# Optimization experiments

Hardware: AMD Instinct MI355X
Metric: run time of the kernel (lower is better)

The kernel has to match this reference:

```python
import jax, jax.numpy as jnp
import numpy as np

EPS = 1e-8

def _cos_loss(a, b):
    # faithful to torch cos_loss: norm = sqrt(sum(x*x)), x / (norm + 1e-8)
    a_norm = jnp.sqrt(jnp.sum(a * a, axis=1, keepdims=True))
    b_norm = jnp.sqrt(jnp.sum(b * b, axis=1, keepdims=True))
    a_n = a / (a_norm + EPS)
    b_n = b / (b_norm + EPS)
    cossim = jnp.sum(a_n * b_n, axis=1)
    return jnp.mean(1.0 - cossim)

def setup_inputs() -> dict:
    key = jax.random.key(0)
    k1, k2, k3 = jax.random.split(key, 3)
    shape = (1, 768, 64, 64)  # [n, c_cat(block2 VGG16 feats), h, w]
    a = jax.random.normal(k1, shape, dtype=jnp.float32)
    b = jax.random.normal(k2, shape, dtype=jnp.float32)
    d = jax.random.normal(k3, shape, dtype=jnp.float32)
    return {"a": a, "b": b, "d": d}

def reference(a, b, d):
    n, c, h, w = a.shape
    hw = h * w
    a_flat = a.reshape(n, c, hw)   # [n, c, hw]
    b_flat = b.reshape(n, c, hw)   # [n, c, h2w2]
    d_flat = d.reshape(n, c, hw)
    # normalize exactly as argmin_cos_distance: sqrt(sum + 1e-8) then /(norm + 1e-8)
    b_norm = jnp.sqrt(jnp.sum(b_flat * b_flat, axis=1, keepdims=True) + EPS)
    b_n = b_flat / (b_norm + EPS)
    a_norm = jnp.sqrt(jnp.sum(a_flat * a_flat, axis=1, keepdims=True) + EPS)
    a_n = a_flat / (a_norm + EPS)
    # cosine distance matrix [n, hw, h2w2]
    d_mat = 1.0 - jnp.einsum('ncp,ncq->npq', a_n, b_n)
    z_best = jnp.argmin(d_mat, axis=2)  # [n, hw]
    # gather matched style features from d
    idx = jnp.broadcast_to(z_best[:, None, :], (n, c, hw))
    target_feats = jnp.take_along_axis(d_flat, idx, axis=2)  # [n, c, hw]
    # NNFM loss between rendered feats and matched style feats (score is detached)
    loss = _cos_loss(a_flat, target_feats)
    z_new = target_feats.reshape(n, c, h, w)
    return (loss, z_new, z_best)
```

## Files before the change

### kernel.cpp

```cpp
#include <hip/hip_runtime.h>
#include <math.h>

#define EPS  1e-8f
#define C    768
#define HW   4096
#define NKB  24
#define NNB  12
#define NBN  32
#define TAU  0.016f
#define NCH_NEW 12
#define NCH_OLD 48

typedef float  floatx4 __attribute__((ext_vector_type(4)));
typedef short  shortx8 __attribute__((ext_vector_type(8)));
typedef unsigned short ushort_t;
typedef unsigned int   uint_t;
typedef __attribute__((address_space(1))) uint_t as1_uint;
typedef __attribute__((address_space(3))) uint_t as3_uint;

__device__ __forceinline__ ushort_t f2bf(float v) {
    uint_t u = __float_as_uint(v);
    uint_t r = (u + 0x7FFFu + ((u >> 16) & 1u)) >> 16;
    return (ushort_t)r;
}
__device__ __forceinline__ void async_cp16(const ushort_t* g, ushort_t* l) {
    __builtin_amdgcn_global_load_lds((const as1_uint*)g, (as3_uint*)l, 16, 0, 0);
}

__global__ __launch_bounds__(256) void prep_kernel(
    const float* __restrict__ a, const float* __restrict__ b,
    const float* __restrict__ d,
    ushort_t* __restrict__ Ah, ushort_t* __restrict__ Bh,
    float* __restrict__ dT, float* __restrict__ bT,
    float* __restrict__ nbp2, float* __restrict__ out)
{
    __shared__ float tile[64][65];
    const int t = threadIdx.x;
    const int p0 = blockIdx.x * 64;
    const int c0 = blockIdx.y * 64;
    const int x = t & 63, y4 = t >> 6;
    const int pl = t >> 2, g = t & 3;
    const int pg = p0 + pl;
    const int sw = (pg >> 1) & 3;

    if (blockIdx.x == 0 && blockIdx.y == 0 && t == 0) out[0] = 0.f;

#pragma unroll
    for (int i = 0; i < 16; ++i) {
        int c = y4 * 16 + i;
        tile[c][x] = d[(size_t)(c0 + c) * HW + p0 + x];
    }
    __syncthreads();
#pragma unroll
    for (int i = 0; i < 16; ++i) {
        int p = y4 * 16 + i;
        dT[(size_t)(p0 + p) * C + c0 + x] = tile[x][p];
    }
    __syncthreads();

#pragma unroll
    for (int i = 0; i < 16; ++i) {
        int c = y4 * 16 + i;
        tile[c][x] = b[(size_t)(c0 + c) * HW + p0 + x];
    }
    __syncthreads();
#pragma unroll
    for (int i = 0; i < 16; ++i) {
        int p = y4 * 16 + i;
        bT[(size_t)(p0 + p) * C + c0 + x] = tile[x][p];
    }
#pragma unroll
    for (int h = 0; h < 2; ++h) {
        const int kb = (c0 >> 5) + h;
        uint_t w[4];
#pragma unroll
        for (int u = 0; u < 4; ++u) {
            ushort_t lo = f2bf(tile[h * 32 + g * 8 + 2 * u][pl]);
            ushort_t hi = f2bf(tile[h * 32 + g * 8 + 2 * u + 1][pl]);
            w[u] = (uint_t)lo | ((uint_t)hi << 16);
        }
        uint4* oh = (uint4*)(Bh + ((size_t)kb * HW + pg) * 32);
        oh[g ^ sw] = make_uint4(w[0], w[1], w[2], w[3]);
    }
    if (t < 64) {
        float s = 0.f;
#pragma unroll
        for (int c = 0; c < 64; ++c) { float v = tile[c][t]; s += v * v; }
        nbp2[blockIdx.y * HW + p0 + t] = s;
    }
    __syncthreads();

#pragma unroll
    for (int i = 0; i < 16; ++i) {
        int c = y4 * 16 + i;
        tile[c][x] = a[(size_t)(c0 + c) * HW + p0 + x];
    }
    __syncthreads();
#pragma unroll
    for (int h = 0; h < 2; ++h) {
        const int kb = (c0 >> 5) + h;
        uint_t w[4];
#pragma unroll
        for (int u = 0; u < 4; ++u) {
            ushort_t lo = f2bf(tile[h * 32 + g * 8 + 2 * u][pl]);
            ushort_t hi = f2bf(tile[h * 32 + g * 8 + 2 * u + 1][pl]);
            w[u] = (uint_t)lo | ((uint_t)hi << 16);
        }
        uint4* oh = (uint4*)(Ah + ((size_t)kb * HW + pg) * 32);
        oh[g ^ sw] = make_uint4(w[0], w[1], w[2], w[3]);
    }
}

__global__ __launch_bounds__(256, 4) void gemm_mfma_kernel(
    const ushort_t* __restrict__ Ah, const ushort_t* __restrict__ Bh,
    const float* __restrict__ nbp2,
    float* __restrict__ pv1, int* __restrict__ pi1,
    float* __restrict__ pv2, int* __restrict__ pi2)
{
    __shared__ __align__(16) char smem[33280];
    ushort_t* sA0 = (ushort_t*)smem;
    ushort_t* sB0 = (ushort_t*)(smem + 8192);
    ushort_t* sA1 = (ushort_t*)(smem + 16384);
    ushort_t* sB1 = (ushort_t*)(smem + 24576);
    float*    nb_s = (float*)(smem + 32768);

    const int tid  = threadIdx.x;
    const int lane = tid & 63;
    const int wave = tid >> 6;
    const int wm = wave >> 1, wn = wave & 1;
    const int bm = blockIdx.x, bn = blockIdx.y;
    const int l15 = lane & 15, l4 = lane >> 4;
    const int swz = (l15 >> 1) & 3;

    floatx4 acc[4][4];
#pragma unroll
    for (int i = 0; i < 4; ++i)
#pragma unroll
        for (int j = 0; j < 4; ++j) acc[i][j] = (floatx4){0.f, 0.f, 0.f, 0.f};

    auto stage = [&](int kb, ushort_t* dA, ushort_t* dB) {
        const size_t aoff = (size_t)(kb * HW + bm * 128) * 32 + tid * 8;
        const size_t boff = (size_t)(kb * HW + bn * 128) * 32 + tid * 8;
        async_cp16(Ah + aoff,        dA + tid * 8);
        async_cp16(Ah + aoff + 2048, dA + tid * 8 + 2048);
        async_cp16(Bh + boff,        dB + tid * 8);
        async_cp16(Bh + boff + 2048, dB + tid * 8 + 2048);
    };
    auto compute = [&](const ushort_t* pA, const ushort_t* pB) {
        shortx8 af[4], bf_[4];
#pragma unroll
        for (int i = 0; i < 4; ++i)
            af[i] = *(const shortx8*)&pA[((wm * 4 + i) * 16 + l15) * 32 + ((l4 ^ swz) * 8)];
#pragma unroll
        for (int j = 0; j < 4; ++j)
            bf_[j] = *(const shortx8*)&pB[((wn * 4 + j) * 16 + l15) * 32 + ((l4 ^ swz) * 8)];
#pragma unroll
        for (int i = 0; i < 4; ++i)
#pragma unroll
            for (int j = 0; j < 4; ++j)
                acc[i][j] = __builtin_amdgcn_mfma_f32_16x16x32_bf16(af[i], bf_[j], acc[i][j], 0, 0, 0);
    };

    stage(0, sA0, sB0);
    if (tid < 128) {
        float s = 0.f;
        int q = bn * 128 + tid;
#pragma unroll
        for (int ch = 0; ch < NNB; ++ch) s += nbp2[ch * HW + q];
        nb_s[tid] = 1.0f / (sqrtf(s + EPS) + EPS);
    }
    __syncthreads();

    for (int kb = 0; kb < NKB; kb += 2) {
        stage(kb + 1, sA1, sB1);
        compute(sA0, sB0);
        __syncthreads();
        if (kb + 2 < NKB) stage(kb + 2, sA0, sB0);
        compute(sA1, sB1);
        __syncthreads();
    }

    float rnb[4];
#pragma unroll
    for (int j = 0; j < 4; ++j)
        rnb[j] = nb_s[wn * 64 + j * 16 + l15];

    float* lv1 = (float*)smem;
    int*   li1 = (int*)(smem + 1024);
    float* lv2 = (float*)(smem + 2048);
    int*   li2 = (int*)(smem + 3072);

#pragma unroll
    for (int i = 0; i < 4; ++i) {
#pragma unroll
        for (int r = 0; r < 4; ++r) {
            float v1 = -INFINITY, v2 = -INFINITY; int i1 = 0, i2 = 0;
#pragma unroll
            for (int j = 0; j < 4; ++j) {
                float sv = acc[i][j][r] * rnb[j];
                int q = bn * 128 + wn * 64 + j * 16 + l15;
                if (sv > v1) { v2 = v1; i2 = i1; v1 = sv; i1 = q; }
                else if (sv > v2) { v2 = sv; i2 = q; }
            }
#pragma unroll
            for (int m = 1; m < 16; m <<= 1) {
                float ov1 = __shfl_xor(v1, m, 64);
                int   oi1 = __shfl_xor(i1, m, 64);
                float ov2 = __shfl_xor(v2, m, 64);
                int   oi2 = __shfl_xor(i2, m, 64);
                if (ov1 > v1 || (ov1 == v1 && oi1 < i1)) {
                    if (v1 > ov2 || (v1 == ov2 && i1 < oi2)) { v2 = v1; i2 = i1; }
                    else { v2 = ov2; i2 = oi2; }
                    v1 = ov1; i1 = oi1;
                } else if (ov1 > v2 || (ov1 == v2 && oi1 < i2)) {
                    v2 = ov1; i2 = oi1;
                }
            }
            if (l15 == 0) {
                int pl = wm * 64 + i * 16 + l4 * 4 + r;
                lv1[pl * 2 + wn] = v1; li1[pl * 2 + wn] = i1;
                lv2[pl * 2 + wn] = v2; li2[pl * 2 + wn] = i2;
            }
        }
    }
    __syncthreads();
    if (tid < 128) {
        float v1 = lv1[tid * 2],     v2 = lv2[tid * 2];
        int   i1 = li1[tid * 2],     i2 = li2[tid * 2];
        float w1 = lv1[tid * 2 + 1], w2 = lv2[tid * 2 + 1];
        int   j1 = li1[tid * 2 + 1], j2 = li2[tid * 2 + 1];
        if (w1 > v1 || (w1 == v1 && j1 < i1)) {
            if (v1 > w2 || (v1 == w2 && i1 < j2)) { v2 = v1; i2 = i1; }
            else { v2 = w2; i2 = j2; }
            v1 = w1; i1 = j1;
        } else if (w1 > v2 || (w1 == v2 && j1 < i2)) {
            v2 = w1; i2 = j1;
        }
        int p = bm * 128 + tid;
        pv1[p * NBN + bn] = v1; pi1[p * NBN + bn] = i1;
        pv2[p * NBN + bn] = v2; pi2[p * NBN + bn] = i2;
    }
}

__global__ __launch_bounds__(256) void reduce_recheck_kernel(
    const float* __restrict__ a, const float* __restrict__ b,
    const float* __restrict__ bT, int bt_ok,
    const float* __restrict__ pv1, const int* __restrict__ pi1,
    const float* __restrict__ pv2, const int* __restrict__ pi2,
    int* __restrict__ zb, float* __restrict__ out_zbest)
{
    const int wave = threadIdx.x >> 6, lane = threadIdx.x & 63;
    const int p = blockIdx.x * 4 + wave;
    const int tq = lane & 31;

    float v1, v2; int i1, cand;
    if (lane < 32) {
        v1 = pv1[p * NBN + tq]; i1 = pi1[p * NBN + tq]; v2 = pv2[p * NBN + tq];
        cand = i1;
    } else {
        v1 = -INFINITY; v2 = -INFINITY; i1 = 0x7fffffff;
        cand = pi2[p * NBN + tq];
    }
#pragma unroll
    for (int m = 1; m < 32; m <<= 1) {
        float ov1 = __shfl_xor(v1, m, 64);
        int   oi1 = __shfl_xor(i1, m, 64);
        float ov2 = __shfl_xor(v2, m, 64);
        if (ov1 > v1 || (ov1 == v1 && oi1 < i1)) {
            v2 = fmaxf(v1, ov2); v1 = ov1; i1 = oi1;
        } else {
            v2 = fmaxf(v2, ov1);
        }
    }
    v1 = __shfl(v1, 0, 64); v2 = __shfl(v2, 0, 64); i1 = __shfl(i1, 0, 64);

    if (v1 - v2 >= TAU) {
        if (lane == 0) { zb[p] = i1; out_zbest[p] = (float)i1; }
        return;
    }

    int q = cand;
    float dot = 0.f, b2 = 0.f;
    if (bt_ok) {
        const float* br = bT + (size_t)q * C;
        const float* ap = a + p;
#pragma unroll 4
        for (int c = 0; c < C; c += 4) {
            float4 bv = *(const float4*)(br + c);
            dot += ap[(size_t)c * HW] * bv.x + ap[(size_t)(c + 1) * HW] * bv.y
                 + ap[(size_t)(c + 2) * HW] * bv.z + ap[(size_t)(c + 3) * HW] * bv.w;
            b2  += bv.x * bv.x + bv.y * bv.y + bv.z * bv.z + bv.w * bv.w;
        }
    } else {
#pragma unroll 8
        for (int c = 0; c < C; ++c) {
            float av = a[c * HW + p];
            float bv = b[c * HW + q];
            dot += av * bv; b2 += bv * bv;
        }
    }
    float s = dot / (sqrtf(b2 + EPS) + EPS);
#pragma unroll
    for (int m = 1; m < 64; m <<= 1) {
        float os = __shfl_xor(s, m, 64);
        int   oq = __shfl_xor(q, m, 64);
        if (os > s || (os == s && oq < q)) { s = os; q = oq; }
    }
    if (lane == 0) { zb[p] = q; out_zbest[p] = (float)q; }
}

__global__ __launch_bounds__(256) void gather_loss_kernel(
    const float* __restrict__ a, const float* __restrict__ dT,
    const int* __restrict__ zb, float* __restrict__ out,
    float* __restrict__ pdot, float* __restrict__ pa2, float* __restrict__ pt2)
{
    __shared__ float tile[64][65];
    __shared__ int qs[64];
    const int t = threadIdx.x;
    const int p0 = blockIdx.x * 64;
    const int c0 = blockIdx.y * 64;
    if (t < 64) qs[t] = zb[p0 + t];
    __syncthreads();

    {
        const int pl = t >> 2, sub = t & 3;
        const float* src = dT + (size_t)qs[pl] * C + c0 + sub * 16;
        float4 v0 = *(const float4*)(src);
        float4 v1 = *(const float4*)(src + 4);
        float4 v2 = *(const float4*)(src + 8);
        float4 v3 = *(const float4*)(src + 12);
        float* dst = &tile[pl][sub * 16];
        dst[0] = v0.x; dst[1] = v0.y; dst[2]  = v0.z; dst[3]  = v0.w;
        dst[4] = v1.x; dst[5] = v1.y; dst[6]  = v1.z; dst[7]  = v1.w;
        dst[8] = v2.x; dst[9] = v2.y; dst[10] = v2.z; dst[11] = v2.w;
        dst[12] = v3.x; dst[13] = v3.y; dst[14] = v3.z; dst[15] = v3.w;
    }
    __syncthreads();

    const int p = t & 63, cg = t >> 6;
    float dot = 0.f, a2 = 0.f, t2 = 0.f;
#pragma unroll
    for (int i = 0; i < 16; ++i) {
        int cc = cg * 16 + i;
        float tv = tile[p][cc];
        float av = a[(size_t)(c0 + cc) * HW + p0 + p];
        out[1 + (size_t)(c0 + cc) * HW + p0 + p] = tv;
        dot += av * tv; a2 += av * av; t2 += tv * tv;
    }
    __shared__ float r1[256], r2[256], r3[256];
    r1[t] = dot; r2[t] = a2; r3[t] = t2;
    __syncthreads();
    if (t < 64) {
        dot = r1[t] + r1[t + 64] + r1[t + 128] + r1[t + 192];
        a2  = r2[t] + r2[t + 64] + r2[t + 128] + r2[t + 192];
        t2  = r3[t] + r3[t + 64] + r3[t + 128] + r3[t + 192];
        pdot[blockIdx.y * HW + p0 + t] = dot;
        pa2[blockIdx.y * HW + p0 + t]  = a2;
        pt2[blockIdx.y * HW + p0 + t]  = t2;
    }
}

__global__ __launch_bounds__(256) void loss_finalize_kernel(
    const float* __restrict__ pdot, const float* __restrict__ pa2,
    const float* __restrict__ pt2, float* __restrict__ out, int nch)
{
    int p = blockIdx.x * 256 + threadIdx.x;
    float dot = 0.f, a2 = 0.f, t2 = 0.f;
#pragma unroll 12
    for (int ch = 0; ch < nch; ++ch) {
        dot += pdot[ch * HW + p];
        a2  += pa2[ch * HW + p];
        t2  += pt2[ch * HW + p];
    }
    float cs = dot / ((sqrtf(a2) + EPS) * (sqrtf(t2) + EPS));
    float contrib = 1.f - cs;
    __shared__ float red[256];
    red[threadIdx.x] = contrib;
    __syncthreads();
    for (int s = 128; s > 0; s >>= 1) {
        if (threadIdx.x < s) red[threadIdx.x] += red[threadIdx.x + s];
        __syncthreads();
    }
    if (threadIdx.x == 0) atomicAdd(out, red[0] * (1.0f / HW));
}

__global__ __launch_bounds__(256) void bnorm_partial_fb_kernel(
    const float* __restrict__ b, float* __restrict__ nbp)
{
    int q = blockIdx.x * 256 + threadIdx.x;
    int c0 = blockIdx.y * 32;
    float s = 0.f;
#pragma unroll 8
    for (int c = c0; c < c0 + 32; ++c) { float v = b[c * HW + q]; s += v * v; }
    nbp[blockIdx.y * HW + q] = s;
}

__global__ __launch_bounds__(256) void bnorm_finalize_fb_kernel(
    const float* __restrict__ nbp, float* __restrict__ nb)
{
    int q = blockIdx.x * 256 + threadIdx.x;
    float s = 0.f;
#pragma unroll
    for (int ch = 0; ch < NKB; ++ch) s += nbp[ch * HW + q];
    nb[q] = sqrtf(s + EPS) + EPS;
}

__global__ __launch_bounds__(256) void gemm_argmax_fb_kernel(
    const float* __restrict__ A, const float* __restrict__ B,
    const float* __restrict__ nb,
    float* __restrict__ pval, int* __restrict__ pidx)
{
    __shared__ __align__(16) char smem[16384];
    float (*As)[128] = (float (*)[128])smem;
    float (*Bs)[128] = (float (*)[128])(smem + 4096);
    const int m0 = blockIdx.x * 128, q0 = blockIdx.y * 128;
    const int tid = threadIdx.x;
    const int tx = tid & 15, ty = tid >> 4;
    const int lr = tid >> 5, lc = (tid & 31) * 4;
    float acc[8][8] = {};
    for (int k0 = 0; k0 < C; k0 += 8) {
        *(float4*)&As[lr][lc] = *(const float4*)&A[(k0 + lr) * HW + m0 + lc];
        *(float4*)&Bs[lr][lc] = *(const float4*)&B[(k0 + lr) * HW + q0 + lc];
        __syncthreads();
#pragma unroll
        for (int kk = 0; kk < 8; ++kk) {
            float a8[8], b8[8];
            *(float4*)&a8[0] = *(float4*)&As[kk][ty * 8];
            *(float4*)&a8[4] = *(float4*)&As[kk][ty * 8 + 4];
            *(float4*)&b8[0] = *(float4*)&Bs[kk][tx * 8];
            *(float4*)&b8[4] = *(float4*)&Bs[kk][tx * 8 + 4];
#pragma unroll
            for (int i = 0; i < 8; ++i)
#pragma unroll
                for (int j = 0; j < 8; ++j) acc[i][j] += a8[i] * b8[j];
        }
        __syncthreads();
    }
    float nbv[8];
#pragma unroll
    for (int j = 0; j < 8; ++j) nbv[j] = nb[q0 + tx * 8 + j];
    float (*rv)[16] = (float (*)[16])smem;
    int   (*ri)[16] = (int   (*)[16])(smem + 8192);
#pragma unroll
    for (int i = 0; i < 8; ++i) {
        float bv = -INFINITY; int bi = 0;
#pragma unroll
        for (int j = 0; j < 8; ++j) {
            float s = acc[i][j] / nbv[j];
            int q = q0 + tx * 8 + j;
            if (s > bv) { bv = s; bi = q; }
        }
        rv[ty * 8 + i][tx] = bv;
        ri[ty * 8 + i][tx] = bi;
    }
    __syncthreads();
    if (tid < 128) {
        float bv = rv[tid][0]; int bi = ri[tid][0];
#pragma unroll
        for (int t = 1; t < 16; ++t) {
            float v = rv[tid][t]; int ii = ri[tid][t];
            if (v > bv || (v == bv && ii < bi)) { bv = v; bi = ii; }
        }
        pval[(m0 + tid) * NBN + blockIdx.y] = bv;
        pidx[(m0 + tid) * NBN + blockIdx.y] = bi;
    }
}

__global__ __launch_bounds__(256) void reduce_fb_kernel(
    const float* __restrict__ pval, const int* __restrict__ pidx,
    int* __restrict__ zb, float* __restrict__ out_zbest)
{
    int p = blockIdx.x * 256 + threadIdx.x;
    float bv = pval[p * NBN]; int bi = pidx[p * NBN];
#pragma unroll 8
    for (int t = 1; t < NBN; ++t) {
        float v = pval[p * NBN + t]; int ii = pidx[p * NBN + t];
        if (v > bv || (v == bv && ii < bi)) { bv = v; bi = ii; }
    }
    zb[p] = bi;
    out_zbest[p] = (float)bi;
}

__global__ __launch_bounds__(256) void gather_partial_kernel(
    const float* __restrict__ a, const float* __restrict__ d,
    const int* __restrict__ zb, float* __restrict__ out,
    float* __restrict__ pdot, float* __restrict__ pa2, float* __restrict__ pt2)
{
    int p = blockIdx.x * 256 + threadIdx.x;
    int ch = blockIdx.y;
    int c0 = ch * (C / NCH_OLD);
    int q = zb[p];
    float dot = 0.f, a2 = 0.f, t2 = 0.f;
#pragma unroll
    for (int c = c0; c < c0 + C / NCH_OLD; ++c) {
        float av = a[c * HW + p];
        float tv = d[c * HW + q];
        dot += av * tv; a2 += av * av; t2 += tv * tv;
        out[1 + c * HW + p] = tv;
    }
    pdot[ch * HW + p] = dot;
    pa2[ch * HW + p] = a2;
    pt2[ch * HW + p] = t2;
}

extern "C" void kernel_launch(void* const* d_in, const int* in_sizes, int n_in,
                              void* d_out, int out_size, void* d_ws, size_t ws_size,
                              hipStream_t stream) {
    const float* a = (const float*)d_in[0];
    const float* b = (const float*)d_in[1];
    const float* d = (const float*)d_in[2];
    float* out = (float*)d_out;
    float* out_zbest = out + 1 + (size_t)C * HW;

    char* ws = (char*)d_ws;
    size_t off = 0;
    auto alloc = [&](size_t bytes) { void* p = ws + off; off = (off + bytes + 255) & ~(size_t)255; return p; };

    const size_t PACK = (size_t)C * HW * 2;
    ushort_t* Ah = (ushort_t*)alloc(PACK);
    ushort_t* Bh = (ushort_t*)alloc(PACK);
    float* nbp = (float*)alloc((size_t)NKB * HW * 4);
    float* pv1 = (float*)alloc((size_t)HW * NBN * 4);
    int*   pi1 = (int*)alloc((size_t)HW * NBN * 4);
    float* pv2 = (float*)alloc((size_t)HW * NBN * 4);
    int*   pi2 = (int*)alloc((size_t)HW * NBN * 4);
    int*   zb  = (int*)alloc(HW * 4);
    float* pdot = (float*)alloc((size_t)NCH_NEW * HW * 4);
    float* pa2  = (float*)alloc((size_t)NCH_NEW * HW * 4);
    float* pt2  = (float*)alloc((size_t)NCH_NEW * HW * 4);
    float* dT  = (float*)alloc((size_t)C * HW * 4);
    float* bT  = (float*)alloc((size_t)C * HW * 4);
    bool fast = off <= ws_size;

    if (fast) {
        prep_kernel<<<dim3(HW / 64, C / 64), 256, 0, stream>>>(
            a, b, d, Ah, Bh, dT, bT, nbp, out);
        gemm_mfma_kernel<<<dim3(HW / 128, HW / 128), 256, 0, stream>>>(
            Ah, Bh, nbp, pv1, pi1, pv2, pi2);
        reduce_recheck_kernel<<<HW / 4, 256, 0, stream>>>(
            a, b, bT, 1, pv1, pi1, pv2, pi2, zb, out_zbest);
        gather_loss_kernel<<<dim3(HW / 64, NCH_NEW), 256, 0, stream>>>(
            a, dT, zb, out, pdot, pa2, pt2);
        loss_finalize_kernel<<<HW / 256, 256, 0, stream>>>(pdot, pa2, pt2, out, NCH_NEW);
    } else {
        off = 0;
        float* nb = (float*)alloc(HW * 4);
        nbp = (float*)alloc((size_t)NKB * HW * 4);
        pv1 = (float*)alloc((size_t)HW * NBN * 4);
        pi1 = (int*)alloc((size_t)HW * NBN * 4);
        zb  = (int*)alloc(HW * 4);
        float* pdot2 = (float*)alloc((size_t)NCH_OLD * HW * 4);
        float* pa22  = (float*)alloc((size_t)NCH_OLD * HW * 4);
        float* pt22  = (float*)alloc((size_t)NCH_OLD * HW * 4);
        hipMemsetAsync(d_out, 0, sizeof(float), stream);
        bnorm_partial_fb_kernel<<<dim3(HW / 256, NKB), 256, 0, stream>>>(b, nbp);
        bnorm_finalize_fb_kernel<<<HW / 256, 256, 0, stream>>>(nbp, nb);
        gemm_argmax_fb_kernel<<<dim3(HW / 128, HW / 128), 256, 0, stream>>>(a, b, nb, pv1, pi1);
        reduce_fb_kernel<<<HW / 256, 256, 0, stream>>>(pv1, pi1, zb, out_zbest);
        gather_partial_kernel<<<dim3(HW / 256, NCH_OLD), 256, 0, stream>>>(
            a, d, zb, out, pdot2, pa22, pt22);
        loss_finalize_kernel<<<HW / 256, 256, 0, stream>>>(pdot2, pa22, pt22, out, NCH_OLD);
    }
}
```

Baseline: 180.2 us.

## Vectorize prep transposes, swizzle GEMM block order, vectorize loss finalize

Result: no change. 180.0 us (-0.1%).

```diff
diff --git a/kernel.cpp b/kernel.cpp
--- a/kernel.cpp
+++ b/kernel.cpp
@@ -38,7 +38,8 @@
     const int t = threadIdx.x;
     const int p0 = blockIdx.x * 64;
     const int c0 = blockIdx.y * 64;
-    const int x = t & 63, y4 = t >> 6;
+    const int r16 = t >> 4;
+    const int q4  = (t & 15) * 4;
     const int pl = t >> 2, g = t & 3;
     const int pg = p0 + pl;
     const int sw = (pg >> 1) & 3;
@@ -46,28 +47,38 @@
     if (blockIdx.x == 0 && blockIdx.y == 0 && t == 0) out[0] = 0.f;
 
 #pragma unroll
-    for (int i = 0; i < 16; ++i) {
-        int c = y4 * 16 + i;
-        tile[c][x] = d[(size_t)(c0 + c) * HW + p0 + x];
-    }
-    __syncthreads();
-#pragma unroll
-    for (int i = 0; i < 16; ++i) {
-        int p = y4 * 16 + i;
-        dT[(size_t)(p0 + p) * C + c0 + x] = tile[x][p];
-    }
-    __syncthreads();
-
-#pragma unroll
-    for (int i = 0; i < 16; ++i) {
-        int c = y4 * 16 + i;
-        tile[c][x] = b[(size_t)(c0 + c) * HW + p0 + x];
-    }
-    __syncthreads();
-#pragma unroll
-    for (int i = 0; i < 16; ++i) {
-        int p = y4 * 16 + i;
-        bT[(size_t)(p0 + p) * C + c0 + x] = tile[x][p];
+    for (int pp = 0; pp < 4; ++pp) {
+        int c = pp * 16 + r16;
+        float4 v = *(const float4*)&d[(size_t)(c0 + c) * HW + p0 + q4];
+        tile[c][q4]     = v.x; tile[c][q4 + 1] = v.y;
+        tile[c][q4 + 2] = v.z; tile[c][q4 + 3] = v.w;
+    }
+    __syncthreads();
+#pragma unroll
+    for (int pp = 0; pp < 4; ++pp) {
+        int p = pp * 16 + r16;
+        float4 v;
+        v.x = tile[q4][p];     v.y = tile[q4 + 1][p];
+        v.z = tile[q4 + 2][p]; v.w = tile[q4 + 3][p];
+        *(float4*)&dT[(size_t)(p0 + p) * C + c0 + q4] = v;
+    }
+    __syncthreads();
+
+#pragma unroll
+    for (int pp = 0; pp < 4; ++pp) {
+        int c = pp * 16 + r16;
+        float4 v = *(const float4*)&b[(size_t)(c0 + c) * HW + p0 + q4];
+        tile[c][q4]     = v.x; tile[c][q4 + 1] = v.y;
+        tile[c][q4 + 2] = v.z; tile[c][q4 + 3] = v.w;
+    }
+    __syncthreads();
+#pragma unroll
+    for (int pp = 0; pp < 4; ++pp) {
+        int p = pp * 16 + r16;
+        float4 v;
+        v.x = tile[q4][p];     v.y = tile[q4 + 1][p];
+        v.z = tile[q4 + 2][p]; v.w = tile[q4 + 3][p];
+        *(float4*)&bT[(size_t)(p0 + p) * C + c0 + q4] = v;
     }
 #pragma unroll
     for (int h = 0; h < 2; ++h) {
@@ -91,9 +102,11 @@
     __syncthreads();
 
 #pragma unroll
-    for (int i = 0; i < 16; ++i) {
-        int c = y4 * 16 + i;
-        tile[c][x] = a[(size_t)(c0 + c) * HW + p0 + x];
+    for (int pp = 0; pp < 4; ++pp) {
+        int c = pp * 16 + r16;
+        float4 v = *(const float4*)&a[(size_t)(c0 + c) * HW + p0 + q4];
+        tile[c][q4]     = v.x; tile[c][q4 + 1] = v.y;
+        tile[c][q4 + 2] = v.z; tile[c][q4 + 3] = v.w;
     }
     __syncthreads();
 #pragma unroll
@@ -128,7 +141,9 @@
     const int lane = tid & 63;
     const int wave = tid >> 6;
     const int wm = wave >> 1, wn = wave & 1;
-    const int bm = blockIdx.x, bn = blockIdx.y;
+    const int flat = blockIdx.y * (HW / 128) + blockIdx.x;
+    const int orig = (flat & 7) * 128 + (flat >> 3);
+    const int bm = orig >> 5, bn = orig & 31;
     const int l15 = lane & 15, l4 = lane >> 4;
     const int swz = (l15 >> 1) & 3;
 
@@ -364,16 +379,23 @@
     const float* __restrict__ pdot, const float* __restrict__ pa2,
     const float* __restrict__ pt2, float* __restrict__ out, int nch)
 {
-    int p = blockIdx.x * 256 + threadIdx.x;
-    float dot = 0.f, a2 = 0.f, t2 = 0.f;
-#pragma unroll 12
+    int p4 = (blockIdx.x * 256 + threadIdx.x) * 4;
+    float d0 = 0.f, d1 = 0.f, d2 = 0.f, d3 = 0.f;
+    float a0 = 0.f, a1 = 0.f, a2 = 0.f, a3 = 0.f;
+    float t0 = 0.f, t1 = 0.f, t2 = 0.f, t3 = 0.f;
     for (int ch = 0; ch < nch; ++ch) {
-        dot += pdot[ch * HW + p];
-        a2  += pa2[ch * HW + p];
-        t2  += pt2[ch * HW + p];
-    }
-    float cs = dot / ((sqrtf(a2) + EPS) * (sqrtf(t2) + EPS));
-    float contrib = 1.f - cs;
+        float4 dv = *(const float4*)&pdot[(size_t)ch * HW + p4];
+        float4 av = *(const float4*)&pa2[(size_t)ch * HW + p4];
+        float4 tv = *(const float4*)&pt2[(size_t)ch * HW + p4];
+        d0 += dv.x; d1 += dv.y; d2 += dv.z; d3 += dv.w;
+        a0 += av.x; a1 += av.y; a2 += av.z; a3 += av.w;
+        t0 += tv.x; t1 += tv.y; t2 += tv.z; t3 += tv.w;
+    }
+    float contrib =
+        (1.f - d0 / ((sqrtf(a0) + EPS) * (sqrtf(t0) + EPS))) +
+        (1.f - d1 / ((sqrtf(a1) + EPS) * (sqrtf(t1) + EPS))) +
+        (1.f - d2 / ((sqrtf(a2) + EPS) * (sqrtf(t2) + EPS))) +
+        (1.f - d3 / ((sqrtf(a3) + EPS) * (sqrtf(t3) + EPS)));
     __shared__ float red[256];
     red[threadIdx.x] = contrib;
     __syncthreads();
@@ -541,7 +563,7 @@
             a, b, bT, 1, pv1, pi1, pv2, pi2, zb, out_zbest);
         gather_loss_kernel<<<dim3(HW / 64, NCH_NEW), 256, 0, stream>>>(
             a, dT, zb, out, pdot, pa2, pt2);
-        loss_finalize_kernel<<<HW / 256, 256, 0, stream>>>(pdot, pa2, pt2, out, NCH_NEW);
+        loss_finalize_kernel<<<HW / 1024, 256, 0, stream>>>(pdot, pa2, pt2, out, NCH_NEW);
     } else {
         off = 0;
         float* nb = (float*)alloc(HW * 4);
@@ -559,6 +581,6 @@
         reduce_fb_kernel<<<HW / 256, 256, 0, stream>>>(pv1, pi1, zb, out_zbest);
         gather_partial_kernel<<<dim3(HW / 256, NCH_OLD), 256, 0, stream>>>(
             a, d, zb, out, pdot2, pa22, pt22);
-        loss_finalize_kernel<<<HW / 256, 256, 0, stream>>>(pdot2, pa22, pt22, out, NCH_OLD);
-    }
-}
+        loss_finalize_kernel<<<HW / 1024, 256, 0, stream>>>(pdot2, pa22, pt22, out, NCH_OLD);
+    }
+}
```
